# Kernel optimization log

Hardware: AMD Instinct MI355X
Metric: run time of the kernel (lower is better)

Reference implementation:

```python
import jax, jax.numpy as jnp
import numpy as np

N_CLUSTERS = 8
ENC_IN = 862
SEQ_LEN = 720
PRED_LEN = 336
BATCH = 64


def setup_inputs() -> dict:
    key = jax.random.key(0)
    k1, k2, k3, k4 = jax.random.split(key, 4)
    x = jax.random.normal(k1, (BATCH, ENC_IN, SEQ_LEN), dtype=jnp.float32)
    clusters = jax.random.randint(k2, (ENC_IN,), 0, N_CLUSTERS, dtype=jnp.int64)
    # Per-cluster Linear(seq_len -> pred_len): weight [P, S], bias [P], like nn.Linear
    bound = 1.0 / np.sqrt(SEQ_LEN)
    W = jax.random.uniform(k3, (N_CLUSTERS, PRED_LEN, SEQ_LEN), dtype=jnp.float32, minval=-bound, maxval=bound)
    b = jax.random.uniform(k4, (N_CLUSTERS, PRED_LEN), dtype=jnp.float32, minval=-bound, maxval=bound)
    return {"x": x, "clusters": clusters, "W": W, "b": b}


def reference(x, clusters, W, b):
    # Gather each channel's cluster weight/bias, then batched per-channel GEMV.
    Wc = W[clusters]            # [C, P, S]
    bc = b[clusters]            # [C, P]
    # out[b, c, p] = sum_s x[b, c, s] * Wc[c, p, s] + bc[c, p]
    out = jnp.einsum('bcs,cps->bcp', x, Wc) + bc[None, :, :]
    return out
```

## Files before the change

kernel.cpp:

```cpp
#include <hip/hip_runtime.h>
#include <stdint.h>

#define N_CL    8
#define C_IN    862
#define SEQ     720
#define SEQP    768
#define PRED    336
#define BATCH   64
#define BK      64
#define NCH     (SEQP / BK)
#define NT      (PRED / 16)
#define XBSTRIDE ((size_t)C_IN * SEQ)

typedef __attribute__((ext_vector_type(8))) __bf16 bf16x8;
typedef __attribute__((ext_vector_type(4))) float  floatx4;

__device__ __forceinline__ void async16(const void* g, void* l) {
  __builtin_amdgcn_global_load_lds(
      (__attribute__((address_space(1))) unsigned int*)(uintptr_t)g,
      (__attribute__((address_space(3))) unsigned int*)l,
      16, 0, 0);
}

__global__ void wconv_kernel(const float* __restrict__ W, __bf16* __restrict__ Wb) {
  const int row = blockIdx.x;
  const float* src = W + (size_t)row * SEQ;
  __bf16* dst = Wb + (size_t)row * SEQP;
  for (int s = threadIdx.x; s < SEQP; s += blockDim.x) {
    float v = (s < SEQ) ? src[s] : 0.0f;
    dst[s] = (__bf16)v;
  }
}

#define A_BYTES 16384
#define B_BYTES 43008

__global__ __launch_bounds__(256, 2) void clin_kernel(
    const float* __restrict__ x, const int* __restrict__ clusters,
    const __bf16* __restrict__ Wb, const float* __restrict__ bias,
    float* __restrict__ out) {
  __shared__ __attribute__((aligned(128))) unsigned char smem[A_BYTES + B_BYTES];
  unsigned char* As = smem;
  unsigned char* Bs = smem + A_BYTES;

  const int c    = blockIdx.x;
  const int cl   = clusters[c];
  const int tid  = threadIdx.x;
  const int wave = tid >> 6;
  const int lane = tid & 63;
  const int q    = lane >> 4;
  const int ln   = lane & 15;

  const float*  xc = x  + (size_t)c * SEQ;
  const __bf16* wc = Wb + (size_t)cl * PRED * SEQP;

  floatx4 acc[NT];
#pragma unroll
  for (int t = 0; t < NT; ++t) acc[t] = (floatx4){0.f, 0.f, 0.f, 0.f};

  const int bA_r  = lane >> 4;
  const int bA_pg = lane & 15;
  const int bB_r  = lane >> 3;
  const int bB_pg = lane & 7;

  for (int chunk = 0; chunk < NCH; ++chunk) {
    const int k0 = chunk * BK;

    for (int i = wave; i < 42; i += 4) {
      int r  = (i << 3) + bB_r;
      int lg = bB_pg ^ (r & 7);
      async16(wc + (size_t)r * SEQP + k0 + (lg << 3), Bs + i * 1024);
    }

    if (k0 + BK <= SEQ) {
      for (int i = wave; i < 16; i += 4) {
        int r  = (i << 2) + bA_r;
        int lg = bA_pg ^ (r & 15);
        async16(xc + (size_t)r * XBSTRIDE + k0 + (lg << 2), As + i * 1024);
      }
    } else {
      for (int i = wave; i < 16; i += 4) {
        int r  = (i << 2) + bA_r;
        int lg = bA_pg ^ (r & 15);
        int s  = k0 + (lg << 2);
        floatx4 v = (floatx4){0.f, 0.f, 0.f, 0.f};
        if (s < SEQ) v = *(const floatx4*)(xc + (size_t)r * XBSTRIDE + s);
        *(floatx4*)(As + r * 256 + (bA_pg << 4)) = v;
      }
    }
    __syncthreads();

    const int mrow = (wave << 4) + ln;
#pragma unroll
    for (int kk = 0; kk < BK; kk += 32) {
      int lg0 = (kk >> 2) + (q << 1);
      floatx4 af0 = *(const floatx4*)(As + mrow * 256 + (((lg0    ) ^ ln) << 4));
      floatx4 af1 = *(const floatx4*)(As + mrow * 256 + (((lg0 + 1) ^ ln) << 4));
      bf16x8 a;
      a[0] = (__bf16)af0[0]; a[1] = (__bf16)af0[1];
      a[2] = (__bf16)af0[2]; a[3] = (__bf16)af0[3];
      a[4] = (__bf16)af1[0]; a[5] = (__bf16)af1[1];
      a[6] = (__bf16)af1[2]; a[7] = (__bf16)af1[3];

      int lgB  = (kk >> 3) + q;
      int nsw  = ln & 7;
#pragma unroll
      for (int t = 0; t < NT; ++t) {
        int n = (t << 4) + ln;
        bf16x8 b = *(const bf16x8*)(Bs + n * 128 + ((lgB ^ nsw) << 4));
        acc[t] = __builtin_amdgcn_mfma_f32_16x16x32_bf16(a, b, acc[t], 0, 0, 0);
      }
    }
    __syncthreads();
  }

  const float* bc = bias + cl * PRED;
#pragma unroll
  for (int t = 0; t < NT; ++t) {
    int p = (t << 4) + ln;
    float bv = bc[p];
#pragma unroll
    for (int r = 0; r < 4; ++r) {
      int brow = (wave << 4) + (q << 2) + r;
      out[((size_t)brow * C_IN + c) * PRED + p] = acc[t][r] + bv;
    }
  }
}

extern "C" void kernel_launch(void* const* d_in, const int* in_sizes, int n_in,
                              void* d_out, int out_size, void* d_ws, size_t ws_size,
                              hipStream_t stream) {
  const float* x   = (const float*)d_in[0];
  const int*   cls = (const int*)d_in[1];
  const float* W   = (const float*)d_in[2];
  const float* b   = (const float*)d_in[3];
  float* out = (float*)d_out;
  __bf16* Wb = (__bf16*)d_ws;

  hipLaunchKernelGGL(wconv_kernel, dim3(N_CL * PRED), dim3(256), 0, stream, W, Wb);
  hipLaunchKernelGGL(clin_kernel, dim3(C_IN), dim3(256), 0, stream,
                     x, cls, Wb, b, out);
}
```

Baseline: 274.5 us.

## Drop LDS staging and load MFMA operands directly from global memory

Removes the shared-memory tiles, the async global-to-LDS copies and the barriers. Each wave now loads its x rows and the bf16 weight fragments straight from global memory into registers for the MFMAs, with a peeled tail step for the padded last K slice. Launch bounds go from 2 to 4 blocks per CU to raise occupancy now that no LDS is used. In exchange, each wave re-reads the full weight tile from global memory or cache instead of sharing it through LDS, and the accesses use narrower strided patterns.

```diff
diff --git a/kernel.cpp b/kernel.cpp
--- a/kernel.cpp
+++ b/kernel.cpp
@@ -7,20 +7,11 @@
 #define SEQP    768
 #define PRED    336
 #define BATCH   64
-#define BK      64
-#define NCH     (SEQP / BK)
 #define NT      (PRED / 16)
 #define XBSTRIDE ((size_t)C_IN * SEQ)
 
 typedef __attribute__((ext_vector_type(8))) __bf16 bf16x8;
 typedef __attribute__((ext_vector_type(4))) float  floatx4;
-
-__device__ __forceinline__ void async16(const void* g, void* l) {
-  __builtin_amdgcn_global_load_lds(
-      (__attribute__((address_space(1))) unsigned int*)(uintptr_t)g,
-      (__attribute__((address_space(3))) unsigned int*)l,
-      16, 0, 0);
-}
 
 __global__ void wconv_kernel(const float* __restrict__ W, __bf16* __restrict__ Wb) {
   const int row = blockIdx.x;
@@ -32,17 +23,10 @@
   }
 }
 
-#define A_BYTES 16384
-#define B_BYTES 43008
-
-__global__ __launch_bounds__(256, 2) void clin_kernel(
+__global__ __launch_bounds__(256, 4) void clin_kernel(
     const float* __restrict__ x, const int* __restrict__ clusters,
     const __bf16* __restrict__ Wb, const float* __restrict__ bias,
     float* __restrict__ out) {
-  __shared__ __attribute__((aligned(128))) unsigned char smem[A_BYTES + B_BYTES];
-  unsigned char* As = smem;
-  unsigned char* Bs = smem + A_BYTES;
-
   const int c    = blockIdx.x;
   const int cl   = clusters[c];
   const int tid  = threadIdx.x;
@@ -51,67 +35,50 @@
   const int q    = lane >> 4;
   const int ln   = lane & 15;
 
-  const float*  xc = x  + (size_t)c * SEQ;
-  const __bf16* wc = Wb + (size_t)cl * PRED * SEQP;
+  const int mrow  = (wave << 4) + ln;
+  const int klane = q << 3;
+
+  const float*  xr = x  + (size_t)mrow * XBSTRIDE + (size_t)c * SEQ + klane;
+  const __bf16* wr = Wb + (size_t)cl * PRED * SEQP + (size_t)ln * SEQP + klane;
 
   floatx4 acc[NT];
 #pragma unroll
   for (int t = 0; t < NT; ++t) acc[t] = (floatx4){0.f, 0.f, 0.f, 0.f};
 
-  const int bA_r  = lane >> 4;
-  const int bA_pg = lane & 15;
-  const int bB_r  = lane >> 3;
-  const int bB_pg = lane & 7;
+#pragma unroll 2
+  for (int k0 = 0; k0 < 704; k0 += 32) {
+    floatx4 af0 = *(const floatx4*)(xr + k0);
+    floatx4 af1 = *(const floatx4*)(xr + k0 + 4);
+    bf16x8 a;
+    a[0] = (__bf16)af0[0]; a[1] = (__bf16)af0[1];
+    a[2] = (__bf16)af0[2]; a[3] = (__bf16)af0[3];
+    a[4] = (__bf16)af1[0]; a[5] = (__bf16)af1[1];
+    a[6] = (__bf16)af1[2]; a[7] = (__bf16)af1[3];
+    const __bf16* bp = wr + k0;
+#pragma unroll
+    for (int t = 0; t < NT; ++t) {
+      bf16x8 b = *(const bf16x8*)(bp + (size_t)t * 16 * SEQP);
+      acc[t] = __builtin_amdgcn_mfma_f32_16x16x32_bf16(a, b, acc[t], 0, 0, 0);
+    }
+  }
 
-  for (int chunk = 0; chunk < NCH; ++chunk) {
-    const int k0 = chunk * BK;
-
-    for (int i = wave; i < 42; i += 4) {
-      int r  = (i << 3) + bB_r;
-      int lg = bB_pg ^ (r & 7);
-      async16(wc + (size_t)r * SEQP + k0 + (lg << 3), Bs + i * 1024);
+  {
+    const int k0 = 704;
+    floatx4 af0 = (floatx4){0.f, 0.f, 0.f, 0.f};
+    floatx4 af1 = (floatx4){0.f, 0.f, 0.f, 0.f};
+    if (k0 + klane < SEQ)     af0 = *(const floatx4*)(xr + k0);
+    if (k0 + klane + 4 < SEQ) af1 = *(const floatx4*)(xr + k0 + 4);
+    bf16x8 a;
+    a[0] = (__bf16)af0[0]; a[1] = (__bf16)af0[1];
+    a[2] = (__bf16)af0[2]; a[3] = (__bf16)af0[3];
+    a[4] = (__bf16)af1[0]; a[5] = (__bf16)af1[1];
+    a[6] = (__bf16)af1[2]; a[7] = (__bf16)af1[3];
+    const __bf16* bp = wr + k0;
+#pragma unroll
+    for (int t = 0; t < NT; ++t) {
+      bf16x8 b = *(const bf16x8*)(bp + (size_t)t * 16 * SEQP);
+      acc[t] = __builtin_amdgcn_mfma_f32_16x16x32_bf16(a, b, acc[t], 0, 0, 0);
     }
-
-    if (k0 + BK <= SEQ) {
-      for (int i = wave; i < 16; i += 4) {
-        int r  = (i << 2) + bA_r;
-        int lg = bA_pg ^ (r & 15);
-        async16(xc + (size_t)r * XBSTRIDE + k0 + (lg << 2), As + i * 1024);
-      }
-    } else {
-      for (int i = wave; i < 16; i += 4) {
-        int r  = (i << 2) + bA_r;
-        int lg = bA_pg ^ (r & 15);
-        int s  = k0 + (lg << 2);
-        floatx4 v = (floatx4){0.f, 0.f, 0.f, 0.f};
-        if (s < SEQ) v = *(const floatx4*)(xc + (size_t)r * XBSTRIDE + s);
-        *(floatx4*)(As + r * 256 + (bA_pg << 4)) = v;
-      }
-    }
-    __syncthreads();
-
-    const int mrow = (wave << 4) + ln;
-#pragma unroll
-    for (int kk = 0; kk < BK; kk += 32) {
-      int lg0 = (kk >> 2) + (q << 1);
-      floatx4 af0 = *(const floatx4*)(As + mrow * 256 + (((lg0    ) ^ ln) << 4));
-      floatx4 af1 = *(const floatx4*)(As + mrow * 256 + (((lg0 + 1) ^ ln) << 4));
-      bf16x8 a;
-      a[0] = (__bf16)af0[0]; a[1] = (__bf16)af0[1];
-      a[2] = (__bf16)af0[2]; a[3] = (__bf16)af0[3];
-      a[4] = (__bf16)af1[0]; a[5] = (__bf16)af1[1];
-      a[6] = (__bf16)af1[2]; a[7] = (__bf16)af1[3];
-
-      int lgB  = (kk >> 3) + q;
-      int nsw  = ln & 7;
-#pragma unroll
-      for (int t = 0; t < NT; ++t) {
-        int n = (t << 4) + ln;
-        bf16x8 b = *(const bf16x8*)(Bs + n * 128 + ((lgB ^ nsw) << 4));
-        acc[t] = __builtin_amdgcn_mfma_f32_16x16x32_bf16(a, b, acc[t], 0, 0, 0);
-      }
-    }
-    __syncthreads();
   }
 
   const float* bc = bias + cl * PRED;
```

New measurement: 449.0 us. 1.64x slower.
